# Kernel optimization log

Measured on AMD Instinct MI355X. Metric: run time of the kernel, lower is better.

## Reference

```python
import jax, jax.numpy as jnp
import numpy as np
from jax import lax

NAG = 3          # hardcoded in the torch module (query slices, catted_torches)
B = 4096         # batch_size per agent
H = 128          # hidden_dim
HEADS = 8
AD = H // HEADS  # attend_dim
STATE, ACT, SCAN = 48, 2, 256
OUTF, HID = 10, 256
NFEAT = 32 * (SCAN - 6)  # conv output features (two VALID convs: k5 then k3)
EPS = 1e-5

def leaky(x):
    return jnp.where(x >= 0, x, 0.01 * x)

def setup_inputs() -> dict:
    key = jax.random.key(0)
    ks = iter(jax.random.split(key, 40))
    def rn(shape, scale=0.05):
        return jax.random.normal(next(ks), shape, dtype=jnp.float32) * scale
    return {
        'obs':  jax.random.normal(next(ks), (NAG * B, STATE), jnp.float32),
        'acts': jax.random.normal(next(ks), (NAG * B, ACT), jnp.float32),
        'scan': jax.random.normal(next(ks), (NAG * B, SCAN), jnp.float32),
        'conv_w1': rn((32, 1, 5)),  'conv_b1': jnp.zeros((32,), jnp.float32),
        'conv_w2': rn((32, 32, 3)), 'conv_b2': jnp.zeros((32,), jnp.float32),
        'fc_w1': rn((256, NFEAT), 0.01), 'fc_b1': jnp.zeros((256,), jnp.float32),
        'fc_w2': rn((OUTF, 256)),        'fc_b2': jnp.zeros((OUTF,), jnp.float32),
        'enc_w': rn((H, STATE + ACT + OUTF)), 'enc_b': jnp.zeros((H,), jnp.float32),
        'Wk': rn((HEADS, AD, H)),
        'Wv': rn((HEADS, AD, H)), 'bv': jnp.zeros((HEADS, AD), jnp.float32),
        'Wq': rn((NAG, HEADS, AD, H)),
        'q1_w1': rn((HID, 2 * H)), 'q1_b1': jnp.zeros((HID,), jnp.float32),
        'q1_w2': rn((HID, HID)),   'q1_b2': jnp.zeros((HID,), jnp.float32),
        'q1_w3': rn((1, HID)),     'q1_b3': jnp.zeros((1,), jnp.float32),
        'q2_w1': rn((HID, 2 * H)), 'q2_b1': jnp.zeros((HID,), jnp.float32),
        'q2_w2': rn((HID, HID)),   'q2_b2': jnp.zeros((HID,), jnp.float32),
        'q2_w3': rn((1, HID)),     'q2_b3': jnp.zeros((1,), jnp.float32),
    }

def reference(obs, acts, scan, conv_w1, conv_b1, conv_w2, conv_b2,
              fc_w1, fc_b1, fc_w2, fc_b2, enc_w, enc_b, Wk, Wv, bv, Wq,
              q1_w1, q1_b1, q1_w2, q1_b2, q1_w3, q1_b3,
              q2_w1, q2_b1, q2_w2, q2_b2, q2_w3, q2_b3):
    dn = ('NCH', 'OIH', 'NCH')
    x = scan[:, None, :]                                            # [N,1,L]
    x = lax.conv_general_dilated(x, conv_w1, (1,), 'VALID', dimension_numbers=dn)
    x = jax.nn.relu(x + conv_b1[None, :, None])
    x = lax.conv_general_dilated(x, conv_w2, (1,), 'VALID', dimension_numbers=dn)
    x = jax.nn.relu(x + conv_b2[None, :, None])
    x = x.reshape(x.shape[0], -1)                                   # [N, NFEAT]
    x = jax.nn.relu(x @ fc_w1.T + fc_b1)
    feats = x @ fc_w2.T + fc_b2                                     # [N, OUTF]

    inps = jnp.concatenate([obs, acts, feats], axis=1)
    mu, var = inps.mean(0), inps.var(0)                             # BatchNorm1d (train, no affine)
    normed = (inps - mu) / jnp.sqrt(var + EPS)
    sa = leaky(normed @ enc_w.T + enc_b).reshape(NAG, B, H)         # [ag,B,H]

    keys = jnp.einsum('gbh,ndh->ngbd', sa, Wk)                      # [hd,ag,B,ad]
    vals = leaky(jnp.einsum('gbh,ndh->ngbd', sa, Wv) + bv[:, None, None, :])
    q = jnp.einsum('gbh,gndh->gnbd', sa, Wq)                        # [ag,hd,B,ad]

    logits = jnp.einsum('gnbd,nobd->gnbo', q, keys) / np.sqrt(AD)   # [ag,hd,B,ag]
    self_mask = jnp.eye(NAG, dtype=bool)[:, None, None, :]          # exclude own agent
    logits = jnp.where(self_mask, -jnp.inf, logits)
    w = jax.nn.softmax(logits, axis=-1)
    other = jnp.einsum('gnbo,nobd->gnbd', w, vals)                  # [ag,hd,B,ad]
    other = other.transpose(0, 2, 1, 3).reshape(NAG, B, H)          # heads concatenated

    emb = jnp.concatenate([sa, other], axis=2).reshape(NAG * B, 2 * H)

    def mlp(x, w1, b1, w2, b2, w3, b3):
        x = jax.nn.relu(x @ w1.T + b1)
        x = jax.nn.relu(x @ w2.T + b2)
        return x @ w3.T + b3

    q1 = mlp(emb, q1_w1, q1_b1, q1_w2, q1_b2, q1_w3, q1_b3)
    q2 = mlp(emb, q2_w1, q2_b1, q2_w2, q2_b2, q2_w3, q2_b3)
    return (q1, q2)
```

## Files before the change

### kernel.cpp

```cpp
#include <hip/hip_runtime.h>
#include <hip/hip_bf16.h>
#include <cstdint>
#include <cstddef>

typedef unsigned short u16;
typedef __attribute__((ext_vector_type(8))) __bf16 bf16x8;
typedef __attribute__((ext_vector_type(4))) float f32x4;

__device__ __forceinline__ u16 f2b(float f) {
  __hip_bfloat16 h = __float2bfloat16(f);
  return *reinterpret_cast<u16*>(&h);
}
__device__ __forceinline__ uint32_t pk2(float a, float b) {
  __hip_bfloat162 h = __float22bfloat162_rn(make_float2(a, b));
  return *reinterpret_cast<uint32_t*>(&h);
}
__device__ __forceinline__ float b2f(u16 u) {
  union { float f; uint32_t i; } x; x.i = ((uint32_t)u) << 16; return x.f;
}
__device__ __forceinline__ f32x4 mfma16(bf16x8 a, bf16x8 b, f32x4 c) {
  return __builtin_amdgcn_mfma_f32_16x16x32_bf16(a, b, c, 0, 0, 0);
}
__device__ __forceinline__ void async16(const void* g, void* l) {
  __builtin_amdgcn_global_load_lds((const __attribute__((address_space(1))) uint32_t*)g,
                                   (__attribute__((address_space(3))) uint32_t*)l, 16, 0, 0);
}

__global__ __launch_bounds__(256) void w1_perm(const float* __restrict__ w,
                                               u16* __restrict__ o) {
  __shared__ float L[8000];
  int j = blockIdx.x, tid = threadIdx.x;
  for (int i = tid; i < 8000; i += 256) L[i] = w[(size_t)j * 8000 + i];
  __syncthreads();
  for (int i = tid; i < 8000; i += 256) {
    int tt = i >> 5, c2 = i & 31;
    o[(size_t)j * 8000 + i] = f2b(L[c2 * 250 + tt]);
  }
}

struct CvtArgs {
  const float* src[8];
  u16* dst[8];
  int cum[9];
};
__global__ __launch_bounds__(256) void f2b_multi(CvtArgs a, float* stats) {
  int i = blockIdx.x * 256 + threadIdx.x;
  if (blockIdx.x == 0 && threadIdx.x < 128) stats[threadIdx.x] = 0.f;
  int seg = 0;
  #pragma unroll
  for (int s = 1; s < 8; ++s) if (i >= a.cum[s]) seg = s;
  if (i < a.cum[8]) {
    int off = i - a.cum[seg];
    if (seg == 7) {
      int c2 = off / 96, rem = off - c2 * 96, kk = rem >> 5, c1 = rem & 31;
      a.dst[7][off] = f2b(a.src[7][(c2 * 32 + c1) * 3 + kk]);
    } else {
      a.dst[seg][off] = f2b(a.src[seg][off]);
    }
  }
}

__global__ __launch_bounds__(256) void conv_fused(
    const float* __restrict__ scan, const float* __restrict__ cw1,
    const float* __restrict__ cb1, const u16* __restrict__ w2g,
    const float* __restrict__ cb2, u16* __restrict__ x, int row0) {
  __shared__ float s[260];
  __shared__ __align__(16) u16 h1T[258 * 40];
  int tid = threadIdx.x;
  int lrow = blockIdx.x;
  int lane = tid & 63, wv = tid >> 6;
  int l15 = lane & 15, quad = lane >> 4;
  s[tid] = scan[(size_t)(row0 + lrow) * 256 + tid];
  if (tid < 4) s[256 + tid] = 0.f;
  if (tid < 240) h1T[252 * 40 + tid] = 0;
  bf16x8 wfrag[2][3];
  #pragma unroll
  for (int i = 0; i < 2; ++i)
    #pragma unroll
    for (int kk = 0; kk < 3; ++kk)
      wfrag[i][kk] = *(const bf16x8*)&w2g[(i * 16 + l15) * 96 + kk * 32 + quad * 8];
  float bias[2][4];
  #pragma unroll
  for (int i = 0; i < 2; ++i)
    #pragma unroll
    for (int r = 0; r < 4; ++r) bias[i][r] = cb2[i * 16 + quad * 4 + r];
  __syncthreads();
  {
    int cpair = tid & 15, pr = tid >> 4;
    int c0 = cpair * 2;
    float wA[5], wB[5];
    #pragma unroll
    for (int k = 0; k < 5; ++k) { wA[k] = cw1[c0 * 5 + k]; wB[k] = cw1[c0 * 5 + 5 + k]; }
    float bA = cb1[c0], bB = cb1[c0 + 1];
    float sv[20];
    int p0 = pr * 16;
    #pragma unroll
    for (int j = 0; j < 5; ++j) {
      f32x4 v = *(const f32x4*)&s[p0 + 4 * j];
      sv[4 * j] = v[0]; sv[4 * j + 1] = v[1]; sv[4 * j + 2] = v[2]; sv[4 * j + 3] = v[3];
    }
    #pragma unroll
    for (int ii = 0; ii < 16; ++ii) {
      float va = bA, vb = bB;
      #pragma unroll
      for (int k = 0; k < 5; ++k) {
        va += sv[ii + k] * wA[k];
        vb += sv[ii + k] * wB[k];
      }
      int p = p0 + ii;
      if (p < 252) {
        *(uint32_t*)&h1T[p * 40 + c0] = pk2(fmaxf(va, 0.f), fmaxf(vb, 0.f));
      }
    }
  }
  __syncthreads();
  f32x4 zero = {0.f, 0.f, 0.f, 0.f};
  f32x4 acc[4][2];
  #pragma unroll
  for (int jj = 0; jj < 4; ++jj) { acc[jj][0] = zero; acc[jj][1] = zero; }
  #pragma unroll
  for (int kk = 0; kk < 3; ++kk) {
    #pragma unroll
    for (int jj = 0; jj < 4; ++jj) {
      int t = (wv * 4 + jj) * 16 + l15 + kk;
      bf16x8 h = *(const bf16x8*)&h1T[t * 40 + quad * 8];
      acc[jj][0] = mfma16(wfrag[0][kk], h, acc[jj][0]);
      acc[jj][1] = mfma16(wfrag[1][kk], h, acc[jj][1]);
    }
  }
  __syncthreads();
  #pragma unroll
  for (int jj = 0; jj < 4; ++jj) {
    int t = (wv * 4 + jj) * 16 + l15;
    if (t < 250) {
      #pragma unroll
      for (int i = 0; i < 2; ++i) {
        float v0 = fmaxf(acc[jj][i][0] + bias[i][0], 0.f);
        float v1 = fmaxf(acc[jj][i][1] + bias[i][1], 0.f);
        float v2 = fmaxf(acc[jj][i][2] + bias[i][2], 0.f);
        float v3 = fmaxf(acc[jj][i][3] + bias[i][3], 0.f);
        uint2 pr2; pr2.x = pk2(v0, v1); pr2.y = pk2(v2, v3);
        *(uint2*)&h1T[t * 40 + i * 16 + quad * 4] = pr2;
      }
    }
  }
  __syncthreads();
  u16* xr = x + (size_t)lrow * 8000;
  #pragma unroll
  for (int it = 0; it < 4; ++it) {
    int e0 = (it * 256 + tid) * 8;
    if (e0 < 8000) {
      int t = e0 >> 5, c8 = (e0 >> 3) & 3;
      bf16x8 v = *(const bf16x8*)&h1T[t * 40 + c8 * 8];
      *(bf16x8*)&xr[e0] = v;
    }
  }
}

template <int MODE>
__global__ __launch_bounds__(256) void gemm_bt(
    const u16* __restrict__ A, int lda, const u16* __restrict__ W,
    const float* __restrict__ bias, float* __restrict__ outF,
    u16* __restrict__ outB, int ldo, int ksteps, int wq_sel, size_t out_zoff) {
  __shared__ __align__(16) u16 As[128 * 32];
  __shared__ __align__(16) u16 Bs[128 * 32];
  int tid = threadIdx.x;
  int m0 = blockIdx.y * 128, n0 = blockIdx.x * 128;
  if (wq_sel) W += (size_t)(blockIdx.y >> 5) * wq_sel;
  int kbase = blockIdx.z * ksteps * 32;
  if (MODE == 0) outF += (size_t)blockIdx.z * out_zoff;
  const u16* Ap = A + (size_t)m0 * lda + kbase;
  const u16* Wp = W + (size_t)n0 * lda + kbase;
  int lane = tid & 63, wv = tid >> 6;
  int l15 = lane & 15, quad = lane >> 4;
  int wm = (wv >> 1) * 64, wn = (wv & 1) * 64;
  int r0 = tid >> 2, kc = (tid & 3) * 8;
  int r1 = (tid + 256) >> 2;
  f32x4 zero = {0.f, 0.f, 0.f, 0.f};
  f32x4 acc[4][4];
  #pragma unroll
  for (int i = 0; i < 4; ++i)
    #pragma unroll
    for (int j = 0; j < 4; ++j) acc[i][j] = zero;
  for (int ks = 0; ks < ksteps; ++ks) {
    __syncthreads();
    async16(Ap + (size_t)r0 * lda + kc, &As[tid * 8]);
    async16(Wp + (size_t)r0 * lda + kc, &Bs[tid * 8]);
    async16(Ap + (size_t)r1 * lda + kc, &As[(tid + 256) * 8]);
    async16(Wp + (size_t)r1 * lda + kc, &Bs[(tid + 256) * 8]);
    __syncthreads();
    bf16x8 af[4], bfr[4];
    #pragma unroll
    for (int i = 0; i < 4; ++i)
      af[i] = *(const bf16x8*)&As[(wm + i * 16 + l15) * 32 + quad * 8];
    #pragma unroll
    for (int j = 0; j < 4; ++j)
      bfr[j] = *(const bf16x8*)&Bs[(wn + j * 16 + l15) * 32 + quad * 8];
    #pragma unroll
    for (int i = 0; i < 4; ++i)
      #pragma unroll
      for (int j = 0; j < 4; ++j) acc[i][j] = mfma16(af[i], bfr[j], acc[i][j]);
    Ap += 32; Wp += 32;
  }
  #pragma unroll
  for (int i = 0; i < 4; ++i) {
    int mb = m0 + wm + i * 16 + quad * 4;
    #pragma unroll
    for (int j = 0; j < 4; ++j) {
      int n = n0 + wn + j * 16 + l15;
      float bv_ = (MODE == 1 || MODE == 2) ? bias[n] : 0.f;
      #pragma unroll
      for (int r = 0; r < 4; ++r) {
        float v = acc[i][j][r];
        if (MODE == 0) {
          outF[(size_t)(mb + r) * ldo + n] = v;
        } else {
          v += bv_;
          if (MODE == 1) v = fmaxf(v, 0.f);
          if (MODE == 2) v = v >= 0.f ? v : 0.01f * v;
          outB[(size_t)(mb + r) * ldo + n] = f2b(v);
        }
      }
    }
  }
}

__global__ __launch_bounds__(256) void fc2_stats(
    const float* __restrict__ hparts, const float* __restrict__ b1,
    const float* __restrict__ w2, const float* __restrict__ b2,
    const float* __restrict__ obs, const float* __restrict__ acts,
    float* __restrict__ inps, float* __restrict__ stats) {
  __shared__ float hL[32 * 260];
  __shared__ float w2L[10 * 260];
  __shared__ float b1L[256];
  __shared__ float ipL[32 * 61];
  int tid = threadIdx.x, r0 = blockIdx.x * 32;
  b1L[tid] = b1[tid];
  for (int i = tid; i < 2560; i += 256) w2L[(i >> 8) * 260 + (i & 255)] = w2[i];
  for (int i = tid; i < 32 * 48; i += 256) {
    int r = i / 48, f = i - r * 48;
    ipL[r * 61 + f] = obs[(size_t)(r0 + r) * 48 + f];
  }
  if (tid < 64) {
    int r = tid >> 1, f = tid & 1;
    ipL[r * 61 + 48 + f] = acts[(size_t)(r0 + r) * 2 + f];
  }
  __syncthreads();
  const size_t HS = (size_t)12288 * 256;
  for (int i = tid; i < 32 * 256; i += 256) {
    int r = i >> 8, c = i & 255;
    size_t g = (size_t)(r0 + r) * 256 + c;
    float v = b1L[c] + hparts[g] + hparts[g + HS] + hparts[g + 2 * HS] +
              hparts[g + 3 * HS] + hparts[g + 4 * HS];
    hL[r * 260 + c] = fmaxf(v, 0.f);
  }
  __syncthreads();
  {
    int r = tid >> 3, ob = tid & 7;
    for (int o = ob; o < 10; o += 8) {
      float a = 0.f;
      #pragma unroll 8
      for (int c = 0; c < 256; ++c) a += hL[r * 260 + c] * w2L[o * 260 + c];
      ipL[r * 61 + 50 + o] = a + b2[o];
    }
  }
  __syncthreads();
  for (int i = tid; i < 32 * 60; i += 256) {
    int r = i / 60, f = i - r * 60;
    inps[(size_t)(r0 + r) * 64 + f] = ipL[r * 61 + f];
  }
  if (tid < 60) {
    float s = 0.f, s2 = 0.f;
    for (int r = 0; r < 32; ++r) {
      float v = ipL[r * 61 + tid];
      s += v; s2 += v * v;
    }
    atomicAdd(&stats[tid], s);
    atomicAdd(&stats[64 + tid], s2);
  }
}

__global__ __launch_bounds__(256) void enc_kernel(
    const float* __restrict__ inps, const float* __restrict__ stats,
    const float* __restrict__ enc_w, const float* __restrict__ enc_b,
    u16* __restrict__ sab) {
  __shared__ float ewL[128 * 61];
  __shared__ float nrm[32 * 61];
  __shared__ float ebL[128];
  __shared__ float muL[60], ivL[60];
  int tid = threadIdx.x, r0 = blockIdx.x * 32;
  if (tid < 128) ebL[tid] = enc_b[tid];
  if (tid < 60) {
    float s = stats[tid], s2 = stats[64 + tid];
    float mu = s * (1.f / 12288.f);
    float var = s2 * (1.f / 12288.f) - mu * mu;
    muL[tid] = mu;
    ivL[tid] = rsqrtf(var + 1e-5f);
  }
  for (int i = tid; i < 128 * 60; i += 256) {
    int h = i / 60, f = i - h * 60;
    ewL[h * 61 + f] = enc_w[i];
  }
  __syncthreads();
  for (int i = tid; i < 32 * 60; i += 256) {
    int r = i / 60, f = i - r * 60;
    nrm[r * 61 + f] = (inps[(size_t)(r0 + r) * 64 + f] - muL[f]) * ivL[f];
  }
  __syncthreads();
  for (int i = tid; i < 32 * 128; i += 256) {
    int r = i >> 7, h = i & 127;
    float a = ebL[h];
    #pragma unroll 4
    for (int f = 0; f < 60; ++f) a += nrm[r * 61 + f] * ewL[h * 61 + f];
    a = a >= 0.f ? a : 0.01f * a;
    sab[(size_t)(r0 + r) * 128 + h] = f2b(a);
  }
}

__global__ __launch_bounds__(128) void attn_combine(
    const u16* __restrict__ qb, const u16* __restrict__ keysb,
    const u16* __restrict__ valsb, const u16* __restrict__ sab,
    u16* __restrict__ emb) {
  __shared__ float qL[3][128], kL[3][128], vL[3][128];
  __shared__ float lg[3][8][3], wgt[3][8][3];
  int b = blockIdx.x, t = threadIdx.x;
  #pragma unroll
  for (int o = 0; o < 3; ++o) {
    size_t base = (size_t)(o * 4096 + b) * 128 + t;
    qL[o][t] = b2f(qb[base]);
    kL[o][t] = b2f(keysb[base]);
    vL[o][t] = b2f(valsb[base]);
  }
  __syncthreads();
  if (t < 72) {
    int g = t / 24, n = (t / 3) % 8, o = t % 3;
    float a = 0.f;
    #pragma unroll
    for (int d = 0; d < 16; ++d) a += qL[g][n * 16 + d] * kL[o][n * 16 + d];
    lg[g][n][o] = (o == g) ? -1e30f : a * 0.25f;
  }
  __syncthreads();
  if (t < 24) {
    int g = t / 8, n = t % 8;
    float m = fmaxf(fmaxf(lg[g][n][0], lg[g][n][1]), lg[g][n][2]);
    float e0 = expf(lg[g][n][0] - m), e1 = expf(lg[g][n][1] - m),
          e2 = expf(lg[g][n][2] - m);
    float inv = 1.f / (e0 + e1 + e2);
    wgt[g][n][0] = e0 * inv; wgt[g][n][1] = e1 * inv; wgt[g][n][2] = e2 * inv;
  }
  __syncthreads();
  int n = t >> 4, d = t & 15;
  #pragma unroll
  for (int g = 0; g < 3; ++g) {
    float o_ = wgt[g][n][0] * vL[0][n * 16 + d] +
               wgt[g][n][1] * vL[1][n * 16 + d] +
               wgt[g][n][2] * vL[2][n * 16 + d];
    size_t rbase = (size_t)(g * 4096 + b) * 256;
    emb[rbase + 128 + t] = f2b(o_);
    emb[rbase + t] = sab[(size_t)(g * 4096 + b) * 128 + t];
  }
}

__global__ __launch_bounds__(256) void final_dot(
    const u16* __restrict__ t2a, const u16* __restrict__ t2b,
    const float* __restrict__ w3a, const float* __restrict__ b3a,
    const float* __restrict__ w3b, const float* __restrict__ b3b,
    float* __restrict__ out) {
  int wv = threadIdx.x >> 6, lane = threadIdx.x & 63;
  int row = blockIdx.x * 4 + wv;
  float sa_ = 0.f, sb_ = 0.f;
  #pragma unroll
  for (int e = 0; e < 4; ++e) {
    int c = lane * 4 + e;
    sa_ += b2f(t2a[(size_t)row * 256 + c]) * w3a[c];
    sb_ += b2f(t2b[(size_t)row * 256 + c]) * w3b[c];
  }
  #pragma unroll
  for (int off = 32; off; off >>= 1) {
    sa_ += __shfl_down(sa_, off);
    sb_ += __shfl_down(sb_, off);
  }
  if (lane == 0) {
    out[row] = sa_ + b3a[0];
    out[12288 + row] = sb_ + b3b[0];
  }
}

extern "C" void kernel_launch(void* const* d_in, const int* in_sizes, int n_in,
                              void* d_out, int out_size, void* d_ws,
                              size_t ws_size, hipStream_t stream) {
  const float* obs  = (const float*)d_in[0];
  const float* acts = (const float*)d_in[1];
  const float* scan = (const float*)d_in[2];
  const float* cw1  = (const float*)d_in[3];
  const float* cb1  = (const float*)d_in[4];
  const float* cw2  = (const float*)d_in[5];
  const float* cb2  = (const float*)d_in[6];
  const float* fw1  = (const float*)d_in[7];
  const float* fb1  = (const float*)d_in[8];
  const float* fw2  = (const float*)d_in[9];
  const float* fb2  = (const float*)d_in[10];
  const float* encw = (const float*)d_in[11];
  const float* encb = (const float*)d_in[12];
  const float* Wk   = (const float*)d_in[13];
  const float* Wv   = (const float*)d_in[14];
  const float* bv   = (const float*)d_in[15];
  const float* Wq   = (const float*)d_in[16];
  const float* q1w1 = (const float*)d_in[17];
  const float* q1b1 = (const float*)d_in[18];
  const float* q1w2 = (const float*)d_in[19];
  const float* q1b2 = (const float*)d_in[20];
  const float* q1w3 = (const float*)d_in[21];
  const float* q1b3 = (const float*)d_in[22];
  const float* q2w1 = (const float*)d_in[23];
  const float* q2b1 = (const float*)d_in[24];
  const float* q2w2 = (const float*)d_in[25];
  const float* q2b2 = (const float*)d_in[26];
  const float* q2w3 = (const float*)d_in[27];
  const float* q2b3 = (const float*)d_in[28];
  float* out = (float*)d_out;
  char* ws = (char*)d_ws;
  if (ws_size < 166009856u) return;

  u16*   x     = (u16*)(ws + 0);
  u16*   w1b   = (u16*)(ws + 98304000);
  float* hpart = (float*)(ws + 102400000);
  float* stats = (float*)(ws + 165314560);
  u16*   wkb   = (u16*)(ws + 165315584);
  u16*   wvb   = (u16*)(ws + 165348352);
  u16*   wqb   = (u16*)(ws + 165381120);
  u16*   m1a   = (u16*)(ws + 165479424);
  u16*   m2a   = (u16*)(ws + 165610496);
  u16*   m1b   = (u16*)(ws + 165741568);
  u16*   m2b   = (u16*)(ws + 165872640);
  u16*   w2g   = (u16*)(ws + 166003712);
  float* inps  = (float*)(ws + 0);
  u16*   sab   = (u16*)(ws + 3145728);
  u16*   keysb = (u16*)(ws + 6291456);
  u16*   valsb = (u16*)(ws + 9437184);
  u16*   qb    = (u16*)(ws + 12582912);
  u16*   embb  = (u16*)(ws + 15728640);
  u16*   t1a   = (u16*)(ws + 22020096);
  u16*   t2a   = (u16*)(ws + 28311552);
  u16*   t1b   = (u16*)(ws + 34603008);
  u16*   t2b   = (u16*)(ws + 40894464);

  w1_perm<<<256, 256, 0, stream>>>(fw1, w1b);
  CvtArgs ca;
  ca.src[0] = Wk;  ca.src[1] = Wv;  ca.src[2] = Wq;  ca.src[3] = q1w1;
  ca.src[4] = q1w2; ca.src[5] = q2w1; ca.src[6] = q2w2; ca.src[7] = cw2;
  ca.dst[0] = wkb; ca.dst[1] = wvb; ca.dst[2] = wqb; ca.dst[3] = m1a;
  ca.dst[4] = m2a; ca.dst[5] = m1b; ca.dst[6] = m2b; ca.dst[7] = w2g;
  const int sz[8] = {16384, 16384, 49152, 65536, 65536, 65536, 65536, 3072};
  int cum = 0;
  ca.cum[0] = 0;
  for (int i = 0; i < 8; ++i) { cum += sz[i]; ca.cum[i + 1] = cum; }
  f2b_multi<<<(cum + 255) / 256, 256, 0, stream>>>(ca, stats);

  for (int s = 0; s < 2; ++s) {
    conv_fused<<<6144, 256, 0, stream>>>(scan, cw1, cb1, w2g, cb2, x, s * 6144);
    gemm_bt<0><<<dim3(2, 48, 5), 256, 0, stream>>>(
        x, 8000, w1b, nullptr, hpart + (size_t)s * 6144 * 256, nullptr, 256,
        50, 0, (size_t)12288 * 256);
  }
  fc2_stats<<<384, 256, 0, stream>>>(hpart, fb1, fw2, fb2, obs, acts, inps, stats);
  enc_kernel<<<384, 256, 0, stream>>>(inps, stats, encw, encb, sab);
  gemm_bt<3><<<dim3(1, 96, 1), 256, 0, stream>>>(sab, 128, wkb, nullptr, nullptr,
                                                 keysb, 128, 4, 0, 0);
  gemm_bt<2><<<dim3(1, 96, 1), 256, 0, stream>>>(sab, 128, wvb, bv, nullptr,
                                                 valsb, 128, 4, 0, 0);
  gemm_bt<3><<<dim3(1, 96, 1), 256, 0, stream>>>(sab, 128, wqb, nullptr, nullptr,
                                                 qb, 128, 4, 16384, 0);
  attn_combine<<<4096, 128, 0, stream>>>(qb, keysb, valsb, sab, embb);
  gemm_bt<1><<<dim3(2, 96, 1), 256, 0, stream>>>(embb, 256, m1a, q1b1, nullptr,
                                                 t1a, 256, 8, 0, 0);
  gemm_bt<1><<<dim3(2, 96, 1), 256, 0, stream>>>(t1a, 256, m2a, q1b2, nullptr,
                                                 t2a, 256, 8, 0, 0);
  gemm_bt<1><<<dim3(2, 96, 1), 256, 0, stream>>>(embb, 256, m1b, q2b1, nullptr,
                                                 t1b, 256, 8, 0, 0);
  gemm_bt<1><<<dim3(2, 96, 1), 256, 0, stream>>>(t1b, 256, m2b, q2b2, nullptr,
                                                 t2b, 256, 8, 0, 0);
  final_dot<<<3072, 256, 0, stream>>>(t2a, t2b, q1w3, q1b3, q2w3, q2b3, out);
}
```

Baseline: 414.5 us.

## Double-buffer GEMM K-tiles of 64 with XOR-swizzled LDS layout

The bf16 MFMA GEMM now stages 64-wide K tiles in two LDS buffers. The next tile's async global-to-LDS loads are issued before the current tile's MFMAs run, which removes one barrier per step and hides load latency. An XOR swizzle on the 16-byte chunk index is applied when loading, and undone when reading, to cut LDS bank conflicts. Every launch halves its step count to match the larger tile. LDS use grows to 64KB per block, which can lower occupancy.

```diff
diff --git a/kernel.cpp b/kernel.cpp
--- a/kernel.cpp
+++ b/kernel.cpp
@@ -161,46 +161,76 @@
 __global__ __launch_bounds__(256) void gemm_bt(
     const u16* __restrict__ A, int lda, const u16* __restrict__ W,
     const float* __restrict__ bias, float* __restrict__ outF,
-    u16* __restrict__ outB, int ldo, int ksteps, int wq_sel, size_t out_zoff) {
-  __shared__ __align__(16) u16 As[128 * 32];
-  __shared__ __align__(16) u16 Bs[128 * 32];
+    u16* __restrict__ outB, int ldo, int nst, int wq_sel, size_t out_zoff) {
+  __shared__ __align__(16) u16 As[2][128 * 64];
+  __shared__ __align__(16) u16 Bs[2][128 * 64];
   int tid = threadIdx.x;
   int m0 = blockIdx.y * 128, n0 = blockIdx.x * 128;
   if (wq_sel) W += (size_t)(blockIdx.y >> 5) * wq_sel;
-  int kbase = blockIdx.z * ksteps * 32;
+  int kbase = blockIdx.z * nst * 64;
   if (MODE == 0) outF += (size_t)blockIdx.z * out_zoff;
   const u16* Ap = A + (size_t)m0 * lda + kbase;
   const u16* Wp = W + (size_t)n0 * lda + kbase;
   int lane = tid & 63, wv = tid >> 6;
   int l15 = lane & 15, quad = lane >> 4;
   int wm = (wv >> 1) * 64, wn = (wv & 1) * 64;
-  int r0 = tid >> 2, kc = (tid & 3) * 8;
-  int r1 = (tid + 256) >> 2;
   f32x4 zero = {0.f, 0.f, 0.f, 0.f};
   f32x4 acc[4][4];
   #pragma unroll
   for (int i = 0; i < 4; ++i)
     #pragma unroll
     for (int j = 0; j < 4; ++j) acc[i][j] = zero;
-  for (int ks = 0; ks < ksteps; ++ks) {
+
+  int srow[4], soff[4], sdst[4];
+  #pragma unroll
+  for (int it = 0; it < 4; ++it) {
+    int c = it * 256 + tid;
+    int row = c >> 3, slot = c & 7;
+    srow[it] = row;
+    soff[it] = ((slot ^ (row & 7)) * 8);
+    sdst[it] = c * 8;
+  }
+  int rslot[2];
+  rslot[0] = ((quad ^ (l15 & 7)) * 8);
+  rslot[1] = (((4 + quad) ^ (l15 & 7)) * 8);
+
+  #pragma unroll 1
+  for (int st = 0; st < nst; ++st) {
+    if (st == 0) {
+      #pragma unroll
+      for (int it = 0; it < 4; ++it) {
+        async16(Ap + (size_t)srow[it] * lda + soff[it], &As[0][sdst[it]]);
+        async16(Wp + (size_t)srow[it] * lda + soff[it], &Bs[0][sdst[it]]);
+      }
+    }
     __syncthreads();
-    async16(Ap + (size_t)r0 * lda + kc, &As[tid * 8]);
-    async16(Wp + (size_t)r0 * lda + kc, &Bs[tid * 8]);
-    async16(Ap + (size_t)r1 * lda + kc, &As[(tid + 256) * 8]);
-    async16(Wp + (size_t)r1 * lda + kc, &Bs[(tid + 256) * 8]);
-    __syncthreads();
-    bf16x8 af[4], bfr[4];
-    #pragma unroll
-    for (int i = 0; i < 4; ++i)
-      af[i] = *(const bf16x8*)&As[(wm + i * 16 + l15) * 32 + quad * 8];
-    #pragma unroll
-    for (int j = 0; j < 4; ++j)
-      bfr[j] = *(const bf16x8*)&Bs[(wn + j * 16 + l15) * 32 + quad * 8];
-    #pragma unroll
-    for (int i = 0; i < 4; ++i)
-      #pragma unroll
-      for (int j = 0; j < 4; ++j) acc[i][j] = mfma16(af[i], bfr[j], acc[i][j]);
-    Ap += 32; Wp += 32;
+    if (st + 1 < nst) {
+      const u16* An = Ap + (st + 1) * 64;
+      const u16* Wn = Wp + (st + 1) * 64;
+      u16* Ad = &As[(st + 1) & 1][0];
+      u16* Bd = &Bs[(st + 1) & 1][0];
+      #pragma unroll
+      for (int it = 0; it < 4; ++it) {
+        async16(An + (size_t)srow[it] * lda + soff[it], Ad + sdst[it]);
+        async16(Wn + (size_t)srow[it] * lda + soff[it], Bd + sdst[it]);
+      }
+    }
+    const u16* Ab = &As[st & 1][0];
+    const u16* Bb = &Bs[st & 1][0];
+    #pragma unroll
+    for (int s = 0; s < 2; ++s) {
+      bf16x8 af[4], bfr[4];
+      #pragma unroll
+      for (int i = 0; i < 4; ++i)
+        af[i] = *(const bf16x8*)&Ab[(wm + i * 16 + l15) * 64 + rslot[s]];
+      #pragma unroll
+      for (int j = 0; j < 4; ++j)
+        bfr[j] = *(const bf16x8*)&Bb[(wn + j * 16 + l15) * 64 + rslot[s]];
+      #pragma unroll
+      for (int i = 0; i < 4; ++i)
+        #pragma unroll
+        for (int j = 0; j < 4; ++j) acc[i][j] = mfma16(af[i], bfr[j], acc[i][j]);
+    }
   }
   #pragma unroll
   for (int i = 0; i < 4; ++i) {
@@ -461,24 +491,24 @@
     conv_fused<<<6144, 256, 0, stream>>>(scan, cw1, cb1, w2g, cb2, x, s * 6144);
     gemm_bt<0><<<dim3(2, 48, 5), 256, 0, stream>>>(
         x, 8000, w1b, nullptr, hpart + (size_t)s * 6144 * 256, nullptr, 256,
-        50, 0, (size_t)12288 * 256);
+        25, 0, (size_t)12288 * 256);
   }
   fc2_stats<<<384, 256, 0, stream>>>(hpart, fb1, fw2, fb2, obs, acts, inps, stats);
   enc_kernel<<<384, 256, 0, stream>>>(inps, stats, encw, encb, sab);
   gemm_bt<3><<<dim3(1, 96, 1), 256, 0, stream>>>(sab, 128, wkb, nullptr, nullptr,
-                                                 keysb, 128, 4, 0, 0);
+                                                 keysb, 128, 2, 0, 0);
   gemm_bt<2><<<dim3(1, 96, 1), 256, 0, stream>>>(sab, 128, wvb, bv, nullptr,
-                                                 valsb, 128, 4, 0, 0);
+                                                 valsb, 128, 2, 0, 0);
   gemm_bt<3><<<dim3(1, 96, 1), 256, 0, stream>>>(sab, 128, wqb, nullptr, nullptr,
-                                                 qb, 128, 4, 16384, 0);
+                                                 qb, 128, 2, 16384, 0);
   attn_combine<<<4096, 128, 0, stream>>>(qb, keysb, valsb, sab, embb);
   gemm_bt<1><<<dim3(2, 96, 1), 256, 0, stream>>>(embb, 256, m1a, q1b1, nullptr,
-                                                 t1a, 256, 8, 0, 0);
+                                                 t1a, 256, 4, 0, 0);
   gemm_bt<1><<<dim3(2, 96, 1), 256, 0, stream>>>(t1a, 256, m2a, q1b2, nullptr,
-                                                 t2a, 256, 8, 0, 0);
+                                                 t2a, 256, 4, 0, 0);
   gemm_bt<1><<<dim3(2, 96, 1), 256, 0, stream>>>(embb, 256, m1b, q2b1, nullptr,
-                                                 t1b, 256, 8, 0, 0);
+                                                 t1b, 256, 4, 0, 0);
   gemm_bt<1><<<dim3(2, 96, 1), 256, 0, stream>>>(t1b, 256, m2b, q2b2, nullptr,
-                                                 t2b, 256, 8, 0, 0);
+                                                 t2b, 256, 4, 0, 0);
   final_dot<<<3072, 256, 0, stream>>>(t2a, t2b, q1w3, q1b3, q2w3, q2b3, out);
 }
```

After: 379.9 us. 8.4% less time.
